# Performance work log

Hardware: AMD Instinct MI355X
Metric: run time of the kernel (lower is better)

Reference implementation:

```python
import jax, jax.numpy as jnp
import numpy as np

NUM_POINTS = 100000
BATCH = 4096
K = 10


def setup_inputs() -> dict:
    key = jax.random.key(0)
    k1, k2, k3, k4, k5 = jax.random.split(key, 5)
    rays_o = jax.random.normal(k1, (BATCH, 3), dtype=jnp.float32)
    rays_d = jax.random.normal(k2, (BATCH, 3), dtype=jnp.float32)
    xyz = jax.random.normal(k3, (NUM_POINTS, 3), dtype=jnp.float32) * 0.1
    features_dc = jax.random.normal(k4, (NUM_POINTS, 1, 3), dtype=jnp.float32)
    opacity = jax.random.normal(k5, (NUM_POINTS, 1), dtype=jnp.float32)
    return {"rays_o": rays_o, "rays_d": rays_d, "xyz": xyz,
            "features_dc": features_dc, "opacity": opacity}


def reference(rays_o, rays_d, xyz, features_dc, opacity):
    # colors = sigmoid(features[:,0,:]) ; features[:,0,:] == features_dc[:,0,:]
    colors = jax.nn.sigmoid(features_dc[:, 0, :])          # [N,3]
    op = jax.nn.sigmoid(opacity[:, 0])                      # [N]
    ray_centers = rays_o + rays_d * 3.0                     # [B,3]
    # Euclidean cdist via ||a||^2 + ||b||^2 - 2 a.b (matmul form, like torch.cdist p=2)
    sq = (jnp.sum(ray_centers * ray_centers, axis=1)[:, None]
          + jnp.sum(xyz * xyz, axis=1)[None, :]
          - 2.0 * ray_centers @ xyz.T)                      # [B,N]
    distances = jnp.sqrt(jnp.maximum(sq, 0.0))
    # top-K smallest distances per ray
    _, idx = jax.lax.top_k(-distances, K)                   # [B,K]
    d_sel = jnp.take_along_axis(distances, idx, axis=1)     # [B,K]
    w = jnp.exp(-d_sel * 0.1) * op[idx]                     # [B,K]
    w = w / (jnp.sum(w, axis=1, keepdims=True) + 1e-8)
    rgb = jnp.einsum('bk,bkc->bc', w, colors[idx])          # [B,3]
    return rgb
```

## Files before the change

### kernel.cpp

```cpp
#include <hip/hip_runtime.h>
#include <math.h>

#define NPTS   100000
#define NRAYS  4096
#define KTOP   10
#define KMER   12
#define CAP    128
#define LCAP   12

#define PPAIR  4
#define SBLK   49
#define RCS    64
#define RPBS   (NRAYS / RCS)

#define TPAIR  4
#define NPART  64
#define TRAYS  8
#define TGRP   16

typedef float v2f __attribute__((ext_vector_type(2)));

static_assert(SBLK * 2048 >= NPTS, "scan covers all points");
static_assert(TGRP * 2048 <= NPTS, "theta sample within real points");

__device__ __forceinline__ float4 make_center(const float* __restrict__ ro,
                                              const float* __restrict__ rd,
                                              int ray, float w) {
    float ox = ro[3 * ray + 0], oy = ro[3 * ray + 1], oz = ro[3 * ray + 2];
    float dx = rd[3 * ray + 0], dy = rd[3 * ray + 1], dz = rd[3 * ray + 2];
    float cx, cy, cz;
    {
#pragma clang fp contract(off)
        cx = ox + dx * 3.0f;
        cy = oy + dy * 3.0f;
        cz = oz + dz * 3.0f;
    }
    return make_float4(cx, cy, cz, w);
}

__device__ __forceinline__ float sigm(float x) { return 1.0f / (1.0f + expf(-x)); }

__device__ __forceinline__ float rfl(float x) {
    return __int_as_float(__builtin_amdgcn_readfirstlane(__float_as_int(x)));
}

__device__ __forceinline__ v2f score2(v2f px, v2f py, v2f pz, v2f pw,
                                      v2f rx, v2f ry, v2f rz) {
    v2f t = __builtin_elementwise_fma(pz, rz, pw);
    t = __builtin_elementwise_fma(py, ry, t);
    return __builtin_elementwise_fma(px, rx, t);
}

__device__ __forceinline__ unsigned long long mkkey(float sc, int id, bool v) {
    unsigned u = __float_as_uint(sc);
    u = (u & 0x80000000u) ? ~u : (u | 0x80000000u);
    unsigned long long k = ((unsigned long long)u << 32) | (unsigned)(~id);
    return v ? k : 0ull;
}

__global__ __launch_bounds__(256, 2) void theta_kernel(const float* __restrict__ xyz,
                                                       const float* __restrict__ ro,
                                                       const float* __restrict__ rd,
                                                       float4* __restrict__ c4,
                                                       int* __restrict__ cnt) {
    __shared__ float4 rsh[TRAYS];
    __shared__ float  Msh[4][TRAYS][64];
    const int tid = threadIdx.x, wave = tid >> 6, lane = tid & 63;
    const int rbase = blockIdx.x * TRAYS;

    if (tid < TRAYS) rsh[tid] = make_center(ro, rd, rbase + tid, 0.0f);
    __syncthreads();

    float4 rr[TRAYS];
#pragma unroll
    for (int r = 0; r < TRAYS; ++r) rr[r] = rsh[r];

    v2f M[TRAYS];
#pragma unroll
    for (int r = 0; r < TRAYS; ++r) M[r] = (v2f){-INFINITY, -INFINITY};

    v2f pxA[TPAIR], pyA[TPAIR], pzA[TPAIR], pwA[TPAIR];
    v2f pxB[TPAIR], pyB[TPAIR], pzB[TPAIR], pwB[TPAIR];

    auto loadg = [&](v2f* PX, v2f* PY, v2f* PZ, v2f* PW, int g) {
        const int id0 = g * 2048 + wave * 512 + lane;
#pragma unroll
        for (int u = 0; u < TPAIR; ++u) {
            int ia = id0 + (2 * u) * 64, ib = id0 + (2 * u + 1) * 64;
            float xa = xyz[3 * ia + 0], ya = xyz[3 * ia + 1], za = xyz[3 * ia + 2];
            float xb = xyz[3 * ib + 0], yb = xyz[3 * ib + 1], zb = xyz[3 * ib + 2];
            PX[u] = (v2f){xa, xb}; PY[u] = (v2f){ya, yb}; PZ[u] = (v2f){za, zb};
            PW[u] = (v2f){-0.5f * fmaf(xa, xa, fmaf(ya, ya, za * za)),
                          -0.5f * fmaf(xb, xb, fmaf(yb, yb, zb * zb))};
        }
    };
    auto computeg = [&](const v2f* PX, const v2f* PY, const v2f* PZ, const v2f* PW) {
#pragma unroll
        for (int r = 0; r < TRAYS; ++r) {
            const v2f rx = (v2f){rr[r].x, rr[r].x};
            const v2f ry = (v2f){rr[r].y, rr[r].y};
            const v2f rz = (v2f){rr[r].z, rr[r].z};
            v2f m = M[r];
#pragma unroll
            for (int u = 0; u < TPAIR; ++u)
                m = __builtin_elementwise_max(m, score2(PX[u], PY[u], PZ[u], PW[u], rx, ry, rz));
            M[r] = m;
        }
    };

    loadg(pxA, pyA, pzA, pwA, 0);
#pragma unroll 1
    for (int g = 0; g < TGRP; g += 2) {
        loadg(pxB, pyB, pzB, pwB, g + 1);
        computeg(pxA, pyA, pzA, pwA);
        if (g + 2 < TGRP) loadg(pxA, pyA, pzA, pwA, g + 2);
        computeg(pxB, pyB, pzB, pwB);
    }

#pragma unroll
    for (int r = 0; r < TRAYS; ++r)
        Msh[wave][r][lane] = fmaxf(M[r].x, M[r].y);
    __syncthreads();

    if (tid < TRAYS) {
        float vs[KTOP];
#pragma unroll
        for (int j = 0; j < KTOP; ++j) vs[j] = -INFINITY;
#pragma unroll 1
        for (int p = 0; p < NPART; ++p) {
            float v = fmaxf(fmaxf(Msh[0][tid][p], Msh[1][tid][p]),
                            fmaxf(Msh[2][tid][p], Msh[3][tid][p]));
#pragma unroll
            for (int t = KTOP - 1; t >= 1; --t) {
                bool up = v > vs[t - 1], here = v > vs[t];
                vs[t] = up ? vs[t - 1] : (here ? v : vs[t]);
            }
            vs[0] = fmaxf(vs[0], v);
        }
        float4 c = rsh[tid];
        c.w = vs[KTOP - 1];
        c4[rbase + tid] = c;
        cnt[rbase + tid] = 0;
    }
}

__global__ __launch_bounds__(256, 4) void scan_kernel(const float* __restrict__ xyz,
                                                      const float4* __restrict__ c4,
                                                      int* __restrict__ cnt,
                                                      float2* __restrict__ cand) {
    __shared__ float4 lsh[RPBS];
    __shared__ int    lcnt[RPBS];
    __shared__ float2 lbuf[RPBS][LCAP];
    const int pblk = blockIdx.x, rchunk = blockIdx.y;
    const int tid = threadIdx.x, wave = tid >> 6, lane = tid & 63;
    const int rbase = rchunk * RPBS;

    if (tid < RPBS) {
        lsh[tid] = c4[rbase + tid];
        lcnt[tid] = 0;
    }

    const int id0 = pblk * 2048 + wave * 512 + lane;
    v2f px[PPAIR], py[PPAIR], pz[PPAIR], pw[PPAIR];
#pragma unroll
    for (int u = 0; u < PPAIR; ++u) {
        int ia = id0 + (2 * u) * 64, ib = id0 + (2 * u + 1) * 64;
        bool va = ia < NPTS, vb = ib < NPTS;
        int ca = va ? ia : 0, cb = vb ? ib : 0;
        float xa = xyz[3 * ca + 0], ya = xyz[3 * ca + 1], za = xyz[3 * ca + 2];
        float xb = xyz[3 * cb + 0], yb = xyz[3 * cb + 1], zb = xyz[3 * cb + 2];
        px[u] = (v2f){xa, xb}; py[u] = (v2f){ya, yb}; pz[u] = (v2f){za, zb};
        pw[u] = (v2f){va ? -0.5f * fmaf(xa, xa, fmaf(ya, ya, za * za)) : -INFINITY,
                      vb ? -0.5f * fmaf(xb, xb, fmaf(yb, yb, zb * zb)) : -INFINITY};
    }
    __syncthreads();

    auto emit = [&](int r, float sc, int id) {
        int slot = atomicAdd(&lcnt[r], 1);
        float2 e = make_float2(sc, __int_as_float(id));
        if (slot < LCAP) lbuf[r][slot] = e;
        else {
            int gs = atomicAdd(&cnt[rbase + r], 1);
            if (gs < CAP) cand[((rbase + r) << 7) + gs] = e;
        }
    };

    auto do_ray = [&](int r, float4 rp) {
        const float cx = rfl(rp.x), cy = rfl(rp.y);
        const float cz = rfl(rp.z), th = rfl(rp.w);
        const v2f rx = (v2f){cx, cx}, ry = (v2f){cy, cy}, rz = (v2f){cz, cz};
        v2f t0 = score2(px[0], py[0], pz[0], pw[0], rx, ry, rz);
        v2f t1 = score2(px[1], py[1], pz[1], pw[1], rx, ry, rz);
        v2f t2 = score2(px[2], py[2], pz[2], pw[2], rx, ry, rz);
        v2f t3 = score2(px[3], py[3], pz[3], pw[3], rx, ry, rz);
        float m1 = fmaxf(fmaxf(t0.x, t0.y), t1.x);
        float m2 = fmaxf(fmaxf(t1.y, t2.x), t2.y);
        float m3 = fmaxf(fmaxf(t3.x, t3.y), m1);
        float hm = fmaxf(m3, m2);

        if (__ballot(hm >= th)) {
            if (t0.x >= th) emit(r, t0.x, id0 + 0 * 64);
            if (t0.y >= th) emit(r, t0.y, id0 + 1 * 64);
            if (t1.x >= th) emit(r, t1.x, id0 + 2 * 64);
            if (t1.y >= th) emit(r, t1.y, id0 + 3 * 64);
            if (t2.x >= th) emit(r, t2.x, id0 + 4 * 64);
            if (t2.y >= th) emit(r, t2.y, id0 + 5 * 64);
            if (t3.x >= th) emit(r, t3.x, id0 + 6 * 64);
            if (t3.y >= th) emit(r, t3.y, id0 + 7 * 64);
        }
    };

    float4 A0 = lsh[0], A1 = lsh[1], A2 = lsh[2], A3 = lsh[3];
#pragma unroll 1
    for (int rb = 0; rb < RPBS; rb += 8) {
        float4 B0 = lsh[rb + 4], B1 = lsh[rb + 5];
        float4 B2 = lsh[rb + 6], B3 = lsh[rb + 7];
        do_ray(rb + 0, A0); do_ray(rb + 1, A1);
        do_ray(rb + 2, A2); do_ray(rb + 3, A3);
        if (rb + 8 < RPBS) {
            A0 = lsh[rb + 8];  A1 = lsh[rb + 9];
            A2 = lsh[rb + 10]; A3 = lsh[rb + 11];
        }
        do_ray(rb + 4, B0); do_ray(rb + 5, B1);
        do_ray(rb + 6, B2); do_ray(rb + 7, B3);
    }

    __syncthreads();
    if (tid < RPBS) {
        int n = lcnt[tid];
        n = n < LCAP ? n : LCAP;
        if (n > 0) {
            const int rayid = rbase + tid;
            int base = atomicAdd(&cnt[rayid], n);
            for (int j = 0; j < n; ++j) {
                int slot = base + j;
                if (slot < CAP) cand[(rayid << 7) + slot] = lbuf[tid][j];
            }
        }
    }
}

__global__ __launch_bounds__(256) void merge_kernel(const float* __restrict__ ro,
                                                    const float* __restrict__ rd,
                                                    const int* __restrict__ cnt,
                                                    const float2* __restrict__ cand,
                                                    const float* __restrict__ xyz,
                                                    const float* __restrict__ fdc,
                                                    const float* __restrict__ opac,
                                                    float* __restrict__ out) {
    const int wave = threadIdx.x >> 6, lane = threadIdx.x & 63;
    const int ray = blockIdx.x * 4 + wave;

    int n = cnt[ray];
    n = n < CAP ? n : CAP;

    const float2* cl = cand + (ray << 7);
    float2 e0 = cl[lane];
    float2 e1 = cl[64 + lane];
    int id0 = __float_as_int(e0.y), id1 = __float_as_int(e1.y);

    unsigned long long k0 = mkkey(e0.x, id0, lane < n);
    unsigned long long k1 = mkkey(e1.x, id1, lane + 64 < n);

    int sel = -1;
    unsigned long long kl = k0 > k1 ? k0 : k1;
#pragma unroll
    for (int j = 0; j < KMER; ++j) {
        unsigned long long m = kl;
#pragma unroll
        for (int off = 1; off < 64; off <<= 1) {
            unsigned long long o = __shfl_xor(m, off);
            m = m > o ? m : o;
        }
        bool win = (kl == m) && (m != 0ull);
        int wid = (k0 >= k1) ? id0 : id1;
        unsigned long long wmask = __ballot(win);
        int wl = __ffsll(wmask) - 1;
        int bid = __shfl(wid, wl & 63);
        if (m == 0ull) bid = -1;
        if (lane == j) sel = bid;
        if (win) {
            if (k0 >= k1) k0 = 0ull; else k1 = 0ull;
            kl = k0 > k1 ? k0 : k1;
        }
    }

    float ox = ro[3 * ray + 0], oy = ro[3 * ray + 1], oz = ro[3 * ray + 2];
    float dx = rd[3 * ray + 0], dy = rd[3 * ray + 1], dz = rd[3 * ray + 2];
    float cxf, cyf, czf;
    {
#pragma clang fp contract(off)
        cxf = ox + dx * 3.0f;
        cyf = oy + dy * 3.0f;
        czf = oz + dz * 3.0f;
    }
    double Cx = (double)cxf, Cy = (double)cyf, Cz = (double)czf;
    double cn = Cx * Cx + Cy * Cy + Cz * Cz;

    bool valid = (lane < KMER) && (sel >= 0);
    int pid = valid ? sel : 0;
    double X = (double)xyz[3 * pid + 0];
    double Y = (double)xyz[3 * pid + 1];
    double Z = (double)xyz[3 * pid + 2];
    double sq = valid ? (cn + (X * X + Y * Y + Z * Z) - 2.0 * (Cx * X + Cy * Y + Cz * Z))
                      : (double)INFINITY;
    int cid = valid ? sel : 0x7fffffff;

    int rank = 0;
#pragma unroll
    for (int k = 0; k < KMER; ++k) {
        double sk = __shfl(sq, k);
        int    ik = __shfl(cid, k);
        if ((sk < sq) || (sk == sq && ik < cid)) ++rank;
    }

    bool take = valid && (rank < KTOP);
    float w = 0.0f, rr = 0.0f, gg = 0.0f, bb = 0.0f;
    if (take) {
        float dd = sqrtf(fmaxf((float)sq, 0.0f));
        w  = expf(-0.1f * dd) * sigm(opac[pid]);
        rr = w * sigm(fdc[3 * pid + 0]);
        gg = w * sigm(fdc[3 * pid + 1]);
        bb = w * sigm(fdc[3 * pid + 2]);
    }
#pragma unroll
    for (int off = 1; off < 64; off <<= 1) {
        w  += __shfl_xor(w,  off);
        rr += __shfl_xor(rr, off);
        gg += __shfl_xor(gg, off);
        bb += __shfl_xor(bb, off);
    }
    if (lane == 0) {
        float inv = 1.0f / (w + 1e-8f);
        out[3 * ray + 0] = rr * inv;
        out[3 * ray + 1] = gg * inv;
        out[3 * ray + 2] = bb * inv;
    }
}

extern "C" void kernel_launch(void* const* d_in, const int* in_sizes, int n_in,
                              void* d_out, int out_size, void* d_ws, size_t ws_size,
                              hipStream_t stream) {
    const float* rays_o = (const float*)d_in[0];
    const float* rays_d = (const float*)d_in[1];
    const float* xyz    = (const float*)d_in[2];
    const float* fdc    = (const float*)d_in[3];
    const float* opac   = (const float*)d_in[4];
    float* out = (float*)d_out;

    char* w = (char*)d_ws;
    float4* c4   = (float4*)w;   w += (size_t)NRAYS * 16;
    int*    cnt  = (int*)w;      w += (size_t)NRAYS * 4;
    float2* cand = (float2*)w;

    theta_kernel<<<NRAYS / TRAYS, 256, 0, stream>>>(xyz, rays_o, rays_d, c4, cnt);
    scan_kernel<<<dim3(SBLK, RCS), 256, 0, stream>>>(xyz, c4, cnt, cand);
    merge_kernel<<<NRAYS / 4, 256, 0, stream>>>(rays_o, rays_d, cnt, cand, xyz, fdc, opac, out);
}
```

Before: 152.7 us.

## Halve points per scan thread, load ray centers from global, raise occupancy

The scan kernel now holds two point pairs per thread instead of four and launches twice as many point blocks. Ray centers and thresholds are read directly from global memory as uniform values, prefetched four rays ahead, instead of being staged through shared memory. Launch-bound occupancy hints rise for both scan and theta kernels, and theta processes fewer rays per block. The aim is lower register pressure and more waves per CU to hide latency, at the cost of more ray-center loads per point and more blocks contending on the global candidate atomics.

```diff
diff --git a/kernel.cpp b/kernel.cpp
--- a/kernel.cpp
+++ b/kernel.cpp
@@ -8,19 +8,19 @@
 #define CAP    128
 #define LCAP   12
 
-#define PPAIR  4
-#define SBLK   49
+#define PPAIR  2
+#define SBLK   98
 #define RCS    64
 #define RPBS   (NRAYS / RCS)
 
 #define TPAIR  4
 #define NPART  64
-#define TRAYS  8
+#define TRAYS  4
 #define TGRP   16
 
 typedef float v2f __attribute__((ext_vector_type(2)));
 
-static_assert(SBLK * 2048 >= NPTS, "scan covers all points");
+static_assert(SBLK * 1024 >= NPTS, "scan covers all points");
 static_assert(TGRP * 2048 <= NPTS, "theta sample within real points");
 
 __device__ __forceinline__ float4 make_center(const float* __restrict__ ro,
@@ -58,7 +58,7 @@
     return v ? k : 0ull;
 }
 
-__global__ __launch_bounds__(256, 2) void theta_kernel(const float* __restrict__ xyz,
+__global__ __launch_bounds__(256, 3) void theta_kernel(const float* __restrict__ xyz,
                                                        const float* __restrict__ ro,
                                                        const float* __restrict__ rd,
                                                        float4* __restrict__ c4,
@@ -144,23 +144,19 @@
     }
 }
 
-__global__ __launch_bounds__(256, 4) void scan_kernel(const float* __restrict__ xyz,
+__global__ __launch_bounds__(256, 6) void scan_kernel(const float* __restrict__ xyz,
                                                       const float4* __restrict__ c4,
                                                       int* __restrict__ cnt,
                                                       float2* __restrict__ cand) {
-    __shared__ float4 lsh[RPBS];
     __shared__ int    lcnt[RPBS];
     __shared__ float2 lbuf[RPBS][LCAP];
     const int pblk = blockIdx.x, rchunk = blockIdx.y;
     const int tid = threadIdx.x, wave = tid >> 6, lane = tid & 63;
     const int rbase = rchunk * RPBS;
 
-    if (tid < RPBS) {
-        lsh[tid] = c4[rbase + tid];
-        lcnt[tid] = 0;
-    }
-
-    const int id0 = pblk * 2048 + wave * 512 + lane;
+    if (tid < RPBS) lcnt[tid] = 0;
+
+    const int id0 = pblk * 1024 + wave * 256 + lane;
     v2f px[PPAIR], py[PPAIR], pz[PPAIR], pw[PPAIR];
 #pragma unroll
     for (int u = 0; u < PPAIR; ++u) {
@@ -185,44 +181,43 @@
         }
     };
 
-    auto do_ray = [&](int r, float4 rp) {
-        const float cx = rfl(rp.x), cy = rfl(rp.y);
-        const float cz = rfl(rp.z), th = rfl(rp.w);
+    auto do_ray = [&](int r, float cx, float cy, float cz, float th) {
         const v2f rx = (v2f){cx, cx}, ry = (v2f){cy, cy}, rz = (v2f){cz, cz};
         v2f t0 = score2(px[0], py[0], pz[0], pw[0], rx, ry, rz);
         v2f t1 = score2(px[1], py[1], pz[1], pw[1], rx, ry, rz);
-        v2f t2 = score2(px[2], py[2], pz[2], pw[2], rx, ry, rz);
-        v2f t3 = score2(px[3], py[3], pz[3], pw[3], rx, ry, rz);
-        float m1 = fmaxf(fmaxf(t0.x, t0.y), t1.x);
-        float m2 = fmaxf(fmaxf(t1.y, t2.x), t2.y);
-        float m3 = fmaxf(fmaxf(t3.x, t3.y), m1);
-        float hm = fmaxf(m3, m2);
+        float hm = fmaxf(fmaxf(t0.x, t0.y), fmaxf(t1.x, t1.y));
 
         if (__ballot(hm >= th)) {
             if (t0.x >= th) emit(r, t0.x, id0 + 0 * 64);
             if (t0.y >= th) emit(r, t0.y, id0 + 1 * 64);
             if (t1.x >= th) emit(r, t1.x, id0 + 2 * 64);
             if (t1.y >= th) emit(r, t1.y, id0 + 3 * 64);
-            if (t2.x >= th) emit(r, t2.x, id0 + 4 * 64);
-            if (t2.y >= th) emit(r, t2.y, id0 + 5 * 64);
-            if (t3.x >= th) emit(r, t3.x, id0 + 6 * 64);
-            if (t3.y >= th) emit(r, t3.y, id0 + 7 * 64);
         }
     };
 
-    float4 A0 = lsh[0], A1 = lsh[1], A2 = lsh[2], A3 = lsh[3];
+    float qx[4], qy[4], qz[4], qw[4];
+    float nx[4], ny[4], nz[4], nw[4];
+#pragma unroll
+    for (int j = 0; j < 4; ++j) {
+        float4 t = c4[rbase + j];
+        qx[j] = rfl(t.x); qy[j] = rfl(t.y); qz[j] = rfl(t.z); qw[j] = rfl(t.w);
+    }
 #pragma unroll 1
-    for (int rb = 0; rb < RPBS; rb += 8) {
-        float4 B0 = lsh[rb + 4], B1 = lsh[rb + 5];
-        float4 B2 = lsh[rb + 6], B3 = lsh[rb + 7];
-        do_ray(rb + 0, A0); do_ray(rb + 1, A1);
-        do_ray(rb + 2, A2); do_ray(rb + 3, A3);
-        if (rb + 8 < RPBS) {
-            A0 = lsh[rb + 8];  A1 = lsh[rb + 9];
-            A2 = lsh[rb + 10]; A3 = lsh[rb + 11];
-        }
-        do_ray(rb + 4, B0); do_ray(rb + 5, B1);
-        do_ray(rb + 6, B2); do_ray(rb + 7, B3);
+    for (int rb = 0; rb < RPBS; rb += 4) {
+        const bool more = (rb + 4 < RPBS);
+        if (more) {
+#pragma unroll
+            for (int j = 0; j < 4; ++j) {
+                float4 t = c4[rbase + rb + 4 + j];
+                nx[j] = rfl(t.x); ny[j] = rfl(t.y); nz[j] = rfl(t.z); nw[j] = rfl(t.w);
+            }
+        }
+#pragma unroll
+        for (int j = 0; j < 4; ++j) do_ray(rb + j, qx[j], qy[j], qz[j], qw[j]);
+        if (more) {
+#pragma unroll
+            for (int j = 0; j < 4; ++j) { qx[j] = nx[j]; qy[j] = ny[j]; qz[j] = nz[j]; qw[j] = nw[j]; }
+        }
     }
 
     __syncthreads();
```

Result: no change. 154.9 us (+1.4%).
